# Kernel optimization log

Hardware: AMD Instinct MI355X
Metric: run time of the kernel (lower is better)

Reference implementation:

```python
import jax, jax.numpy as jnp
import numpy as np

DEPTH = 8
IN_FEATURES = 512
OUT_FEATURES = 256
LEAF_COUNT = 2 ** DEPTH          # 256
GATE_COUNT = LEAF_COUNT - 1      # 255
BATCH = 65536


def setup_inputs() -> dict:
    key = jax.random.key(0)
    k1, k2, k3 = jax.random.split(key, 3)
    x = jax.random.normal(k1, (BATCH, IN_FEATURES), dtype=jnp.float32)
    # gw stored transposed as (in_features, gate_count), kaiming-like scale
    gw = jax.random.normal(k2, (IN_FEATURES, GATE_COUNT), dtype=jnp.float32) * (1.0 / np.sqrt(IN_FEATURES))
    gb = jnp.zeros((GATE_COUNT,), dtype=jnp.float32)
    z = jax.random.normal(k3, (OUT_FEATURES, LEAF_COUNT), dtype=jnp.float32)
    return {"x": x, "gw": gw, "gb": gb, "z": z}


def _leaf_probs(x, gw, gb):
    # gatings: (B, gate_count); node it's left child (2p+1) uses g, right child (2p+2) uses 1-g
    g = jax.nn.sigmoid(x @ gw + gb)
    B = x.shape[0]
    dens = jnp.ones((B, 1), dtype=x.dtype)
    for d in range(DEPTH):  # level-wise vectorized traversal, O(depth) steps
        lo, hi = 2 ** d - 1, 2 ** (d + 1) - 1
        gl = g[:, lo:hi]  # (B, 2^d) gatings at this level
        # interleave [parent*g, parent*(1-g)] -> children order matches heap layout
        dens = jnp.stack([dens * gl, dens * (1.0 - gl)], axis=-1).reshape(B, -1)
    return dens  # (B, leaf_count)


def reference(x, gw, gb, z):
    leaf = _leaf_probs(x, gw, gb)        # (B, L)
    # constant projection: z @ leaf_probs^T, then transpose -> (B, out)
    return leaf @ z.T
```

## Files before the change

kernel.cpp:

```cpp
#include <hip/hip_runtime.h>
#include <hip/hip_bf16.h>
#include <stdint.h>


typedef short bf16x8 __attribute__((ext_vector_type(8)));
typedef float f32x4  __attribute__((ext_vector_type(4)));

__device__ __forceinline__ unsigned short f2bf(float f) {
    union { float f; uint32_t u; } c; c.f = f;
    uint32_t u = c.u;
    return (unsigned short)((u + 0x7FFFu + ((u >> 16) & 1u)) >> 16);
}

__device__ __forceinline__ uint32_t pkbf(float a, float b) {
    union { __hip_bfloat162 h; uint32_t u; } cv;
    cv.h = __float22bfloat162_rn(make_float2(a, b));
    return cv.u;
}

__global__ __launch_bounds__(256) void softtree_prep(
    const float* __restrict__ gw, const float* __restrict__ z,
    unsigned short* __restrict__ gwt, unsigned short* __restrict__ zb)
{
    if (blockIdx.x < 32) {
        __shared__ float tsm[64][65];
        const int k0 = (blockIdx.x >> 2) * 64;
        const int n0 = (blockIdx.x & 3) * 64;
        const int r = threadIdx.x >> 6;
        const int c = threadIdx.x & 63;
        const int n = n0 + c;
        #pragma unroll
        for (int i = 0; i < 16; ++i) {
            int kk = r + i * 4;
            tsm[kk][c] = (n < 255) ? gw[(size_t)(k0 + kk) * 255 + n] : 0.0f;
        }
        __syncthreads();
        #pragma unroll
        for (int i = 0; i < 16; ++i) {
            int nn = r + i * 4;
            gwt[(size_t)(n0 + nn) * 512 + k0 + c] = f2bf(tsm[c][nn]);
        }
    } else {
        int base = (blockIdx.x - 32) * 1024 + threadIdx.x * 4;
        const float4 v = *(const float4*)(z + base);
        ushort4 o;
        o.x = f2bf(v.x); o.y = f2bf(v.y); o.z = f2bf(v.z); o.w = f2bf(v.w);
        *(ushort4*)(zb + base) = o;
    }
}

__global__ __launch_bounds__(512, 4) void softtree_g(
    const float* __restrict__ x, const float* __restrict__ gb,
    const unsigned short* __restrict__ gwt, float* __restrict__ g)
{
    __shared__ char smraw[81920];

    const int tid  = threadIdx.x;
    const int lane = tid & 63;
    const int wv   = tid >> 6;
    const int q    = lane >> 4;
    const int l15  = lane & 15;
    const int wr   = wv & 3;
    const int wc   = wv >> 2;
    const int R0   = blockIdx.x * 128;

    float gbv[8];
    #pragma unroll
    for (int nt = 0; nt < 8; ++nt) {
        int col = 128 * wc + nt * 16 + l15;
        gbv[nt] = (col < 255) ? gb[col] : 0.0f;
    }
    asm volatile("s_waitcnt vmcnt(0)" ::: "memory");

    const float* xsrc0 = x + (size_t)(R0 + 16 * wv + (lane >> 3)) * 512
                           + (size_t)(((lane & 7) ^ (lane >> 3)) * 4);
    const unsigned short* gsrc0 = gwt + (size_t)(32 * wv + (lane >> 2)) * 512
                                      + (size_t)(((lane & 3) ^ ((lane >> 2) & 3)) * 8);
    const uint32_t xdst = (uint32_t)wv * 2048;
    const uint32_t gdst = 49152u + (uint32_t)wv * 2048;

    #define ISSUE_X(kc, xb)                                                                    \
        do {                                                                                   \
            const float* s_ = xsrc0 + (kc) * 32;                                               \
            __builtin_amdgcn_global_load_lds(                                                  \
                (const __attribute__((address_space(1))) void*)(s_),                           \
                (__attribute__((address_space(3))) void*)(smraw + (xb) * 16384 + xdst),        \
                16, 0, 0);                                                                     \
            __builtin_amdgcn_global_load_lds(                                                  \
                (const __attribute__((address_space(1))) void*)(s_ + 8 * 512),                 \
                (__attribute__((address_space(3))) void*)(smraw + (xb) * 16384 + xdst + 1024), \
                16, 0, 0);                                                                     \
        } while (0)

    #define ISSUE_G(kc, gwb)                                                                   \
        do {                                                                                   \
            const unsigned short* s_ = gsrc0 + (kc) * 32;                                      \
            __builtin_amdgcn_global_load_lds(                                                  \
                (const __attribute__((address_space(1))) void*)(s_),                           \
                (__attribute__((address_space(3))) void*)(smraw + (gwb) * 16384 + gdst),       \
                16, 0, 0);                                                                     \
            __builtin_amdgcn_global_load_lds(                                                  \
                (const __attribute__((address_space(1))) void*)(s_ + 16 * 512),                \
                (__attribute__((address_space(3))) void*)(smraw + (gwb) * 16384 + gdst + 1024),\
                16, 0, 0);                                                                     \
        } while (0)

    f32x4 acc[2][8];
    #pragma unroll
    for (int t = 0; t < 2; ++t)
        #pragma unroll
        for (int i = 0; i < 8; ++i) acc[t][i] = (f32x4){0.f, 0.f, 0.f, 0.f};

    ISSUE_X(0, 0);
    ISSUE_G(0, 0);
    ISSUE_X(1, 1);

    int xb = 0, gwb = 0;
    for (int kc = 0; kc < 15; ++kc) {
        asm volatile("s_waitcnt vmcnt(2)" ::: "memory");
        __builtin_amdgcn_s_barrier();
        __builtin_amdgcn_sched_barrier(0);

        ISSUE_G(kc + 1, gwb ^ 1);
        if (kc < 14) {
            int xb2 = xb + 2; if (xb2 >= 3) xb2 -= 3;
            ISSUE_X(kc + 2, xb2);
        }

        {
            const char* xbase = smraw + xb * 16384;
            const char* gbase = smraw + 49152 + gwb * 16384;
            bf16x8 a[2];
            #pragma unroll
            for (int t = 0; t < 2; ++t) {
                const char* ra = xbase + (64 * t + 16 * wr + l15) * 128;
                f32x4 lo = *(const f32x4*)(ra + (((2 * q)     ^ (l15 & 7)) * 16));
                f32x4 hi = *(const f32x4*)(ra + (((2 * q + 1) ^ (l15 & 7)) * 16));
                union { bf16x8 v; uint32_t u[4]; } pk;
                pk.u[0] = pkbf(lo[0], lo[1]); pk.u[1] = pkbf(lo[2], lo[3]);
                pk.u[2] = pkbf(hi[0], hi[1]); pk.u[3] = pkbf(hi[2], hi[3]);
                a[t] = pk.v;
            }
            __builtin_amdgcn_s_setprio(1);
            #pragma unroll
            for (int nt = 0; nt < 8; ++nt) {
                const bf16x8 b = *(const bf16x8*)(gbase + (128 * wc + nt * 16 + l15) * 64
                                                        + ((q ^ (l15 & 3)) * 16));
                acc[0][nt] = __builtin_amdgcn_mfma_f32_16x16x32_bf16(a[0], b, acc[0][nt], 0, 0, 0);
                acc[1][nt] = __builtin_amdgcn_mfma_f32_16x16x32_bf16(a[1], b, acc[1][nt], 0, 0, 0);
            }
            __builtin_amdgcn_s_setprio(0);
        }

        xb = (xb == 2) ? 0 : xb + 1;
        gwb ^= 1;
    }

    asm volatile("s_waitcnt vmcnt(0)" ::: "memory");
    __builtin_amdgcn_s_barrier();
    __builtin_amdgcn_sched_barrier(0);
    {
        const char* xbase = smraw + xb * 16384;
        const char* gbase = smraw + 49152 + gwb * 16384;
        bf16x8 a[2];
        #pragma unroll
        for (int t = 0; t < 2; ++t) {
            const char* ra = xbase + (64 * t + 16 * wr + l15) * 128;
            f32x4 lo = *(const f32x4*)(ra + (((2 * q)     ^ (l15 & 7)) * 16));
            f32x4 hi = *(const f32x4*)(ra + (((2 * q + 1) ^ (l15 & 7)) * 16));
            union { bf16x8 v; uint32_t u[4]; } pk;
            pk.u[0] = pkbf(lo[0], lo[1]); pk.u[1] = pkbf(lo[2], lo[3]);
            pk.u[2] = pkbf(hi[0], hi[1]); pk.u[3] = pkbf(hi[2], hi[3]);
            a[t] = pk.v;
        }
        __builtin_amdgcn_s_setprio(1);
        #pragma unroll
        for (int nt = 0; nt < 8; ++nt) {
            const bf16x8 b = *(const bf16x8*)(gbase + (128 * wc + nt * 16 + l15) * 64
                                                    + ((q ^ (l15 & 3)) * 16));
            acc[0][nt] = __builtin_amdgcn_mfma_f32_16x16x32_bf16(a[0], b, acc[0][nt], 0, 0, 0);
            acc[1][nt] = __builtin_amdgcn_mfma_f32_16x16x32_bf16(a[1], b, acc[1][nt], 0, 0, 0);
        }
        __builtin_amdgcn_s_setprio(0);
    }

    #undef ISSUE_X
    #undef ISSUE_G

    #pragma unroll
    for (int t = 0; t < 2; ++t) {
        #pragma unroll
        for (int nt = 0; nt < 8; ++nt) {
            const int col = 128 * wc + nt * 16 + l15;
            #pragma unroll
            for (int r = 0; r < 4; ++r) {
                const int row = R0 + t * 64 + 16 * wr + 4 * q + r;
                float v = acc[t][nt][r] + gbv[nt];
                g[(size_t)row * 256 + col] = 1.0f / (1.0f + __expf(-v));
            }
        }
    }
}

__global__ __launch_bounds__(512, 4) void softtree_leaf(
    const float* __restrict__ g, unsigned short* __restrict__ leaf)
{
    __shared__ float gs[64 * 260];

    const int tid  = threadIdx.x;
    const int lane = tid & 63;
    const int q    = lane >> 4;
    const int l15  = lane & 15;
    const int wv   = tid >> 6;
    const int wr   = wv & 3;
    const int R0   = blockIdx.x * 128;

    const int srow = tid >> 3;
    const int scol = (tid & 7) * 32;

    for (int t = 0; t < 2; ++t) {
        if (t) __syncthreads();

        const float* gsrc = g + (size_t)(R0 + 64 * t + srow) * 256 + scol;
        #pragma unroll
        for (int i = 0; i < 8; ++i) {
            f32x4 v = *(const f32x4*)(gsrc + 4 * i);
            *(f32x4*)(gs + srow * 260 + scol + 4 * i) = v;
        }
        __syncthreads();

        const float* gr = gs + (16 * wr + l15) * 260;
        const int row = R0 + 64 * t + 16 * wr + l15;
        float g0v = gr[0];
        float t1v[2] = { g0v, 1.0f - g0v };
        float t2v[4], t3v[8];
        #pragma unroll
        for (int u = 0; u < 2; ++u) {
            float gl = gr[1 + u];
            t2v[2 * u] = t1v[u] * gl; t2v[2 * u + 1] = t1v[u] - t2v[2 * u];
        }
        #pragma unroll
        for (int u = 0; u < 4; ++u) {
            float gl = gr[3 + u];
            t3v[2 * u] = t2v[u] * gl; t3v[2 * u + 1] = t2v[u] - t3v[2 * u];
        }
        #pragma unroll
        for (int c = 0; c < 8; ++c) {
            const int G = c * 4 + q;
            float p = t3v[c];
            float g3 = gr[7 + c];
            p = (q & 2) ? (p - p * g3) : (p * g3);
            float g4 = gr[15 + 2 * c + (q >> 1)];
            p = (q & 1) ? (p - p * g4) : (p * g4);
            float g5 = gr[31 + G];
            float a0 = p * g5, a1 = p - a0;
            float g6a = gr[63 + 2 * G], g6b = gr[64 + 2 * G];
            float b00 = a0 * g6a, b01 = a0 - b00;
            float b10 = a1 * g6b, b11 = a1 - b10;
            float g70 = gr[127 + 4 * G], g71 = gr[128 + 4 * G];
            float g72 = gr[129 + 4 * G], g73 = gr[130 + 4 * G];
            float lf0 = b00 * g70, lf1 = b00 - lf0;
            float lf2 = b01 * g71, lf3 = b01 - lf2;
            float lf4 = b10 * g72, lf5 = b10 - lf4;
            float lf6 = b11 * g73, lf7 = b11 - lf6;
            union { uint4 u4; uint32_t u[4]; } pk;
            pk.u[0] = pkbf(lf0, lf1);
            pk.u[1] = pkbf(lf2, lf3);
            pk.u[2] = pkbf(lf4, lf5);
            pk.u[3] = pkbf(lf6, lf7);
            *(uint4*)(leaf + (size_t)row * 256 + 32 * c + 8 * q) = pk.u4;
        }
    }
}

__global__ __launch_bounds__(512, 4) void softtree_out(
    const unsigned short* __restrict__ leaf, const unsigned short* __restrict__ zb,
    float* __restrict__ out)
{
    __shared__ char smraw[57344];

    const int tid  = threadIdx.x;
    const int lane = tid & 63;
    const int wv   = tid >> 6;
    const int q    = lane >> 4;
    const int l15  = lane & 15;
    const int wr   = wv & 3;
    const int wc   = wv >> 2;
    const int R0   = blockIdx.x * 128;

    const unsigned short* lsrc0 = leaf + (size_t)(R0 + 16 * wv + (lane >> 2)) * 256
                                       + (size_t)(((lane & 3) ^ ((lane >> 2) & 3)) * 8);
    const unsigned short* zsrc0 = zb + (size_t)(32 * wv + (lane >> 2)) * 256
                                     + (size_t)(((lane & 3) ^ ((lane >> 2) & 3)) * 8);
    const uint32_t ldst = (uint32_t)wv * 1024;
    const uint32_t zdst = 24576u + (uint32_t)wv * 2048;

    #define ISSUE_L(kc, lb_)                                                                   \
        __builtin_amdgcn_global_load_lds(                                                      \
            (const __attribute__((address_space(1))) void*)(lsrc0 + (kc) * 32),                \
            (__attribute__((address_space(3))) void*)(smraw + (lb_) * 8192 + ldst),            \
            16, 0, 0)

    #define ISSUE_Z(kc, zb_)                                                                   \
        do {                                                                                   \
            const unsigned short* s_ = zsrc0 + (kc) * 32;                                      \
            __builtin_amdgcn_global_load_lds(                                                  \
                (const __attribute__((address_space(1))) void*)(s_),                           \
                (__attribute__((address_space(3))) void*)(smraw + (zb_) * 16384 + zdst),       \
                16, 0, 0);                                                                     \
            __builtin_amdgcn_global_load_lds(                                                  \
                (const __attribute__((address_space(1))) void*)(s_ + 4096),                    \
                (__attribute__((address_space(3))) void*)(smraw + (zb_) * 16384 + zdst + 1024),\
                16, 0, 0);                                                                     \
        } while (0)

    f32x4 acc[2][8];
    #pragma unroll
    for (int t = 0; t < 2; ++t)
        #pragma unroll
        for (int i = 0; i < 8; ++i) acc[t][i] = (f32x4){0.f, 0.f, 0.f, 0.f};

    ISSUE_L(0, 0);
    ISSUE_Z(0, 0);
    ISSUE_L(1, 1);

    int lb = 0, zbuf = 0;
    for (int kc = 0; kc < 7; ++kc) {
        asm volatile("s_waitcnt vmcnt(1)" ::: "memory");
        __builtin_amdgcn_s_barrier();
        __builtin_amdgcn_sched_barrier(0);

        ISSUE_Z(kc + 1, zbuf ^ 1);
        if (kc < 6) {
            int lb2 = lb + 2; if (lb2 >= 3) lb2 -= 3;
            ISSUE_L(kc + 2, lb2);
        }

        {
            const char* lbase = smraw + lb * 8192;
            const char* zbase = smraw + 24576 + zbuf * 16384;
            bf16x8 a[2];
            #pragma unroll
            for (int t = 0; t < 2; ++t)
                a[t] = *(const bf16x8*)(lbase + (((64 * t + 16 * wr + l15) * 4
                                                  + (q ^ (l15 & 3))) * 16));
            __builtin_amdgcn_s_setprio(1);
            #pragma unroll
            for (int nt = 0; nt < 8; ++nt) {
                const int n = 128 * wc + nt * 16 + l15;
                const bf16x8 b = *(const bf16x8*)(zbase + ((n * 4 + (q ^ (l15 & 3))) * 16));
                acc[0][nt] = __builtin_amdgcn_mfma_f32_16x16x32_bf16(a[0], b, acc[0][nt], 0, 0, 0);
                acc[1][nt] = __builtin_amdgcn_mfma_f32_16x16x32_bf16(a[1], b, acc[1][nt], 0, 0, 0);
            }
            __builtin_amdgcn_s_setprio(0);
        }

        lb = (lb == 2) ? 0 : lb + 1;
        zbuf ^= 1;
    }

    asm volatile("s_waitcnt vmcnt(0)" ::: "memory");
    __builtin_amdgcn_s_barrier();
    __builtin_amdgcn_sched_barrier(0);
    {
        const char* lbase = smraw + lb * 8192;
        const char* zbase = smraw + 24576 + zbuf * 16384;
        bf16x8 a[2];
        #pragma unroll
        for (int t = 0; t < 2; ++t)
            a[t] = *(const bf16x8*)(lbase + (((64 * t + 16 * wr + l15) * 4
                                              + (q ^ (l15 & 3))) * 16));
        __builtin_amdgcn_s_setprio(1);
        #pragma unroll
        for (int nt = 0; nt < 8; ++nt) {
            const int n = 128 * wc + nt * 16 + l15;
            const bf16x8 b = *(const bf16x8*)(zbase + ((n * 4 + (q ^ (l15 & 3))) * 16));
            acc[0][nt] = __builtin_amdgcn_mfma_f32_16x16x32_bf16(a[0], b, acc[0][nt], 0, 0, 0);
            acc[1][nt] = __builtin_amdgcn_mfma_f32_16x16x32_bf16(a[1], b, acc[1][nt], 0, 0, 0);
        }
        __builtin_amdgcn_s_setprio(0);
    }

    #undef ISSUE_L
    #undef ISSUE_Z

    #pragma unroll
    for (int t = 0; t < 2; ++t) {
        #pragma unroll
        for (int nt = 0; nt < 8; ++nt) {
            const int col = 128 * wc + nt * 16 + l15;
            #pragma unroll
            for (int r = 0; r < 4; ++r) {
                const int row = R0 + t * 64 + 16 * wr + 4 * q + r;
                out[(size_t)row * 256 + col] = acc[t][nt][r];
            }
        }
    }
}

extern "C" void kernel_launch(void* const* d_in, const int* in_sizes, int n_in,
                              void* d_out, int out_size, void* d_ws, size_t ws_size,
                              hipStream_t stream) {
    const float* x  = (const float*)d_in[0];
    const float* gw = (const float*)d_in[1];
    const float* gb = (const float*)d_in[2];
    const float* z  = (const float*)d_in[3];
    float* outp = (float*)d_out;

    unsigned short* gwt  = (unsigned short*)d_ws;
    unsigned short* zbf  = gwt + 256 * 512;
    float*          gbuf = (float*)((char*)d_ws + (1u << 20));
    unsigned short* leaf = (unsigned short*)((char*)d_ws + 70u * (1u << 20));

    softtree_prep<<<96, 256, 0, stream>>>(gw, z, gwt, zbf);
    softtree_g<<<512, 512, 0, stream>>>(x, gb, gwt, gbuf);
    softtree_leaf<<<512, 512, 0, stream>>>(gbuf, leaf);
    softtree_out<<<512, 512, 0, stream>>>(leaf, zbf, outp);
}
```

Baseline: 275.5 us.

## Fuse gating GEMM and leaf-probability kernels via shared-memory handoff

Merges the gating GEMM+sigmoid kernel with the leaf-probability kernel, so sigmoid outputs go to shared memory instead of a 64 MB global fp32 buffer that was then read back. Each block computes leaf probabilities for its own 128 rows, with all 8 waves splitting the leaf columns (4 chunks each) to use the extra waves. This removes a full global write/read round trip and one kernel launch. In exchange it adds block barriers and a smaller shared-memory stride (258), which may cause bank conflicts.

```diff
diff --git a/kernel.cpp b/kernel.cpp
--- a/kernel.cpp
+++ b/kernel.cpp
@@ -49,11 +49,12 @@
     }
 }
 
-__global__ __launch_bounds__(512, 4) void softtree_g(
+__global__ __launch_bounds__(512, 4) void softtree_gleaf(
     const float* __restrict__ x, const float* __restrict__ gb,
-    const unsigned short* __restrict__ gwt, float* __restrict__ g)
+    const unsigned short* __restrict__ gwt, unsigned short* __restrict__ leaf)
 {
     __shared__ char smraw[81920];
+    float* gs = (float*)smraw;
 
     const int tid  = threadIdx.x;
     const int lane = tid & 63;
@@ -187,49 +188,23 @@
     #undef ISSUE_X
     #undef ISSUE_G
 
-    #pragma unroll
+    const int c0 = (wv >> 2) * 4;
     for (int t = 0; t < 2; ++t) {
+        __syncthreads();
+
         #pragma unroll
         for (int nt = 0; nt < 8; ++nt) {
             const int col = 128 * wc + nt * 16 + l15;
             #pragma unroll
             for (int r = 0; r < 4; ++r) {
-                const int row = R0 + t * 64 + 16 * wr + 4 * q + r;
+                const int rowl = 16 * wr + 4 * q + r;
                 float v = acc[t][nt][r] + gbv[nt];
-                g[(size_t)row * 256 + col] = 1.0f / (1.0f + __expf(-v));
-            }
-        }
-    }
-}
-
-__global__ __launch_bounds__(512, 4) void softtree_leaf(
-    const float* __restrict__ g, unsigned short* __restrict__ leaf)
-{
-    __shared__ float gs[64 * 260];
-
-    const int tid  = threadIdx.x;
-    const int lane = tid & 63;
-    const int q    = lane >> 4;
-    const int l15  = lane & 15;
-    const int wv   = tid >> 6;
-    const int wr   = wv & 3;
-    const int R0   = blockIdx.x * 128;
-
-    const int srow = tid >> 3;
-    const int scol = (tid & 7) * 32;
-
-    for (int t = 0; t < 2; ++t) {
-        if (t) __syncthreads();
-
-        const float* gsrc = g + (size_t)(R0 + 64 * t + srow) * 256 + scol;
-        #pragma unroll
-        for (int i = 0; i < 8; ++i) {
-            f32x4 v = *(const f32x4*)(gsrc + 4 * i);
-            *(f32x4*)(gs + srow * 260 + scol + 4 * i) = v;
+                gs[rowl * 258 + col] = 1.0f / (1.0f + __expf(-v));
+            }
         }
         __syncthreads();
 
-        const float* gr = gs + (16 * wr + l15) * 260;
+        const float* gr = gs + (16 * wr + l15) * 258;
         const int row = R0 + 64 * t + 16 * wr + l15;
         float g0v = gr[0];
         float t1v[2] = { g0v, 1.0f - g0v };
@@ -245,7 +220,8 @@
             t3v[2 * u] = t2v[u] * gl; t3v[2 * u + 1] = t2v[u] - t3v[2 * u];
         }
         #pragma unroll
-        for (int c = 0; c < 8; ++c) {
+        for (int ci = 0; ci < 4; ++ci) {
+            const int c = c0 + ci;
             const int G = c * 4 + q;
             float p = t3v[c];
             float g3 = gr[7 + c];
@@ -409,11 +385,9 @@
 
     unsigned short* gwt  = (unsigned short*)d_ws;
     unsigned short* zbf  = gwt + 256 * 512;
-    float*          gbuf = (float*)((char*)d_ws + (1u << 20));
     unsigned short* leaf = (unsigned short*)((char*)d_ws + 70u * (1u << 20));
 
     softtree_prep<<<96, 256, 0, stream>>>(gw, z, gwt, zbf);
-    softtree_g<<<512, 512, 0, stream>>>(x, gb, gwt, gbuf);
-    softtree_leaf<<<512, 512, 0, stream>>>(gbuf, leaf);
+    softtree_gleaf<<<512, 512, 0, stream>>>(x, gb, gwt, leaf);
     softtree_out<<<512, 512, 0, stream>>>(leaf, zbf, outp);
 }
```

Result: faster. 251.1 us (-8.9%).
